# Optimization experiments

Hardware: AMD Instinct MI355X
Metric: run time of the kernel (lower is better)

The kernel has to match this reference:

```python
import jax, jax.numpy as jnp
import numpy as np

# dims: T time steps, B batch, CIN/COUT conv channels, HxW spatial, K kernel
T, B, CIN, COUT, H, Wd, K = 10, 32, 3, 64, 64, 64, 3
DECAY = 0.2      # LIF leak factor
INH = 1.625      # lateral inhibition strength (mode='threshold')


def setup_inputs() -> dict:
    key = jax.random.key(0)
    k1, k2 = jax.random.split(key)
    x = (jax.random.uniform(k1, (T, B, CIN, H, Wd)) < 0.2).astype(jnp.float32)
    W = jax.random.normal(k2, (COUT, CIN, K, K), dtype=jnp.float32)
    # normweight(): zero-mean, unit-std (biased) per output filter
    W = W - W.mean(axis=(1, 2, 3), keepdims=True)
    W = W / W.reshape(COUT, -1).std(axis=1).reshape(COUT, 1, 1, 1)
    return {"x": x, "W": W}


def _conv(x, W):
    # Conv2d stride=1, padding=1, no bias, NCHW/OIHW
    return jax.lax.conv_general_dilated(
        x, W, window_strides=(1, 1), padding=((1, 1), (1, 1)),
        dimension_numbers=("NCHW", "OIHW", "NCHW"))


def reference(x, W):
    def step(mem, x_t):
        i = _conv(x_t, W)                                        # (B,COUT,H,W)
        # ATB: adaptive per-channel threshold = max over batch+spatial
        thr = jnp.max(i, axis=(0, 2, 3), keepdims=True) + 1e-4   # (1,COUT,1,1)
        # ASF: clamp then thresholded sigmoid filter
        cur = jnp.maximum(i, 0.0)
        i_asf = thr * jax.nn.sigmoid((cur - 0.4 * thr) * (8.0 / thr))
        # LIF update with threshold = thr (set by ATB)
        mem = mem * DECAY + i_asf
        s = (mem > thr).astype(mem.dtype)                        # spikes 0/1
        # WTA k=1: keep only the strongest spiking channel per location
        score = mem * s
        winner = jnp.argmax(score, axis=1)                       # (B,H,W)
        oh = jnp.moveaxis(jax.nn.one_hot(winner, COUT, dtype=mem.dtype), -1, 1)
        s = s * oh
        # membrane reset of fired neurons
        mem = mem * (1.0 - s)
        # lateral inhibition: suppress non-winners at spiking locations
        any_sp = jnp.max(s, axis=1, keepdims=True)
        mem = mem - INH * thr * any_sp * (1.0 - s)
        return mem, s

    mem0 = jnp.zeros((B, COUT, H, Wd), jnp.float32)
    _, spikes = jax.lax.scan(step, mem0, x)
    return spikes  # (T,B,COUT,H,W)
```

## Files before the change

kernel.cpp:

```cpp
#include <hip/hip_runtime.h>
#include <math.h>

#define TT 10
#define BB 32
#define CIN 3
#define COUT 64
#define HH 64
#define WW 64
#define HW (HH*WW)
#define DECAY 0.2f
#define INH 1.625f

__device__ __forceinline__ unsigned int enc_f(float f) {
    unsigned int u = __float_as_uint(f);
    return (u & 0x80000000u) ? ~u : (u | 0x80000000u);
}
__device__ __forceinline__ float dec_f(unsigned int u) {
    u = (u & 0x80000000u) ? (u & 0x7FFFFFFFu) : ~u;
    return __uint_as_float(u);
}

__global__ __launch_bounds__(256) void thr_kernel(
    const float* __restrict__ x,
    const float* __restrict__ Wt,
    unsigned int* __restrict__ thr_raw,
    float* __restrict__ out)
{
    __shared__ float sx[CIN][6][68];
    __shared__ float wmax[4][COUT];

    const int tid  = threadIdx.x;
    const int lane = tid & 63;
    const int wave = tid >> 6;
    const int h0   = blockIdx.x * 4;
    const int b    = blockIdx.y;
    const int t    = blockIdx.z;

    float w[27];
    #pragma unroll
    for (int k = 0; k < 27; k++) w[k] = Wt[lane * 27 + k];

    const float* xb = x + ((size_t)t * BB + b) * (CIN * HW);
    for (int l = tid; l < CIN * 6 * 66; l += 256) {
        int ci  = l / 396;
        int r   = (l % 396) / 66;
        int col = l % 66;
        int gh = h0 + r - 1;
        int gw = col - 1;
        float v = 0.f;
        if (gh >= 0 && gh < HH && gw >= 0 && gw < WW)
            v = xb[ci * HW + gh * WW + gw];
        sx[ci][r][col] = v;
    }
    __syncthreads();

    float* ob = out + (((size_t)t * BB + b) * COUT) * HW;
    float mx = -INFINITY;

    for (int cc = 0; cc < 16; cc++) {
        {
            int l   = cc * 256 + tid;
            int row = l >> 4;
            int q   = l & 15;
            int c   = row >> 2;
            int hr  = row & 3;
            *(float4*)(ob + (size_t)c * HW + (h0 + hr) * WW + q * 4) =
                make_float4(0.f, 0.f, 0.f, 0.f);
        }
        float acc0 = 0.f, acc1 = 0.f, acc2 = 0.f, acc3 = 0.f;
        #pragma unroll
        for (int ci = 0; ci < CIN; ci++)
            #pragma unroll
            for (int kh = 0; kh < 3; kh++) {
                const float* rp = &sx[ci][wave + kh][cc * 4];
                float4 q = *(const float4*)rp;
                float2 r2 = *(const float2*)(rp + 4);
                float x0 = q.x, x1 = q.y, x2 = q.z, x3 = q.w;
                float x4 = r2.x, x5 = r2.y;
                const float w0 = w[ci * 9 + kh * 3 + 0];
                const float w1 = w[ci * 9 + kh * 3 + 1];
                const float w2 = w[ci * 9 + kh * 3 + 2];
                acc0 = fmaf(w0, x0, acc0); acc0 = fmaf(w1, x1, acc0); acc0 = fmaf(w2, x2, acc0);
                acc1 = fmaf(w0, x1, acc1); acc1 = fmaf(w1, x2, acc1); acc1 = fmaf(w2, x3, acc1);
                acc2 = fmaf(w0, x2, acc2); acc2 = fmaf(w1, x3, acc2); acc2 = fmaf(w2, x4, acc2);
                acc3 = fmaf(w0, x3, acc3); acc3 = fmaf(w1, x4, acc3); acc3 = fmaf(w2, x5, acc3);
            }
        mx = fmaxf(mx, fmaxf(fmaxf(acc0, acc1), fmaxf(acc2, acc3)));
    }

    wmax[wave][lane] = mx;
    __syncthreads();
    if (wave == 0) {
        float m = fmaxf(fmaxf(wmax[0][lane], wmax[1][lane]),
                        fmaxf(wmax[2][lane], wmax[3][lane]));
        atomicMax(&thr_raw[t * COUT + lane], enc_f(m));
    }
}

__global__ __launch_bounds__(256) void fused_kernel(
    const float* __restrict__ x,
    const float* __restrict__ Wt,
    const unsigned int* __restrict__ thr_raw,
    float* __restrict__ out)
{
    __shared__ float sx[5][CIN][3][24];

    const int tid  = threadIdx.x;
    const int lane = tid & 63;
    const int wave = tid >> 6;
    const int p0   = __builtin_amdgcn_readfirstlane(wave * 4);
    const int b    = blockIdx.x >> 8;
    const int h    = (blockIdx.x >> 2) & 63;
    const int w0   = (blockIdx.x & 3) << 4;

    float w[27];
    #pragma unroll
    for (int k = 0; k < 27; k++) w[k] = Wt[lane * 27 + k];

    const float* xb0 = x + (size_t)b * (CIN * HW);

#define STAGE5(T0) {                                                          \
        for (int l = tid; l < 5 * 162; l += 256) {                            \
            int t   = l / 162;                                                \
            int r0  = l - t * 162;                                            \
            int ci  = r0 / 54;                                                \
            int r1  = r0 - ci * 54;                                           \
            int r   = r1 / 18;                                                \
            int col = r1 - r * 18;                                            \
            int gh = h + r - 1;                                               \
            int gw = w0 + col - 1;                                            \
            float v = 0.f;                                                    \
            if (gh >= 0 && gh < HH && gw >= 0 && gw < WW)                     \
                v = xb0[(size_t)((T0) + t) * ((size_t)BB * CIN * HW)          \
                        + ci * HW + gh * WW + gw];                            \
            sx[t][ci][r][col] = v;                                            \
        }                                                                     \
    }

    STAGE5(0);

    float mem[4];
    #pragma unroll
    for (int j = 0; j < 4; j++) mem[j] = 0.f;

    __syncthreads();

    #pragma unroll 1
    for (int t = 0; t < TT; t++) {
        if (t == 5) {
            __syncthreads();
            STAGE5(5);
            __syncthreads();
        }
        const int slot = (t < 5) ? t : t - 5;

        float thr   = dec_f(thr_raw[t * COUT + lane]) + 1e-4f;
        float sinv  = 8.0f / thr;
        float s04   = 0.4f * thr;
        float sinh_ = INH * thr;

        int fmask = 0;

        float acc0 = 0.f, acc1 = 0.f, acc2 = 0.f, acc3 = 0.f;
        #pragma unroll
        for (int ci = 0; ci < CIN; ci++)
            #pragma unroll
            for (int kh = 0; kh < 3; kh++) {
                const float* rp = &sx[slot][ci][kh][p0];
                float4 q = *(const float4*)rp;
                float2 r2 = *(const float2*)(rp + 4);
                float x0 = q.x, x1 = q.y, x2 = q.z, x3 = q.w;
                float x4 = r2.x, x5 = r2.y;
                const float w0_ = w[ci * 9 + kh * 3 + 0];
                const float w1_ = w[ci * 9 + kh * 3 + 1];
                const float w2_ = w[ci * 9 + kh * 3 + 2];
                acc0 = fmaf(w0_, x0, acc0); acc0 = fmaf(w1_, x1, acc0); acc0 = fmaf(w2_, x2, acc0);
                acc1 = fmaf(w0_, x1, acc1); acc1 = fmaf(w1_, x2, acc1); acc1 = fmaf(w2_, x3, acc1);
                acc2 = fmaf(w0_, x2, acc2); acc2 = fmaf(w1_, x3, acc2); acc2 = fmaf(w2_, x4, acc2);
                acc3 = fmaf(w0_, x3, acc3); acc3 = fmaf(w1_, x4, acc3); acc3 = fmaf(w2_, x5, acc3);
            }

#define LIF_PX(J, ACC) {                                                    \
        float cur = fmaxf(ACC, 0.f);                                        \
        float z   = (cur - s04) * sinv;                                     \
        float sig = 1.0f / (1.0f + expf(-z));                               \
        float m   = mem[J] * DECAY + thr * sig;                             \
        int   sp  = m > thr;                                                \
        float score = sp ? m : 0.f;                                         \
        unsigned long long blt = __ballot(sp);                              \
        int fr = 0, sp_any = 0;                                             \
        if (blt) {                                  \
            float bs = score;                                               \
            int   bc = lane;                                                \
            _Pragma("unroll")                                               \
            for (int off = 32; off > 0; off >>= 1) {                        \
                float so = __shfl_xor(bs, off, 64);                         \
                int   co = __shfl_xor(bc, off, 64);                         \
                if (so > bs || (so == bs && co < bc)) { bs = so; bc = co; } \
            }                                                               \
            int spw = __shfl(sp, bc, 64);      \
            fr     = (lane == bc) && sp;                                    \
            sp_any = spw;                                                   \
        }                                                                   \
        mem[J] = fr ? 0.f : (m - (sp_any ? sinh_ : 0.f));                   \
        if (fr) fmask |= (1 << (J));                                        \
    }

        LIF_PX(0, acc0);
        LIF_PX(1, acc1);
        LIF_PX(2, acc2);
        LIF_PX(3, acc3);
#undef LIF_PX

        if (fmask) {
            float* os = out + (((size_t)t * BB + b) * COUT) * HW + h * WW + w0;
            #pragma unroll
            for (int j = 0; j < 4; j++)
                if (fmask & (1 << j))
                    os[(size_t)lane * HW + p0 + j] = 1.0f;
        }
    }
#undef STAGE5
}

extern "C" void kernel_launch(void* const* d_in, const int* in_sizes, int n_in,
                              void* d_out, int out_size, void* d_ws, size_t ws_size,
                              hipStream_t stream) {
    const float* x = (const float*)d_in[0];
    const float* W = (const float*)d_in[1];
    float* out     = (float*)d_out;

    unsigned int* thr = (unsigned int*)d_ws;
    hipMemsetAsync(thr, 0, TT * COUT * sizeof(unsigned int), stream);

    thr_kernel<<<dim3(HH / 4, BB, TT), 256, 0, stream>>>(x, W, thr, out);
    fused_kernel<<<dim3(BB * HH * 4), 256, 0, stream>>>(x, W, thr, out);
}
```

Measured before the change: 518.9 us.

## Fuse threshold and LIF passes into one cooperative kernel with grid sync

```diff
diff --git a/kernel.cpp b/kernel.cpp
--- a/kernel.cpp
+++ b/kernel.cpp
@@ -1,5 +1,8 @@
 #include <hip/hip_runtime.h>
+#include <hip/hip_cooperative_groups.h>
 #include <math.h>
+
+namespace cg = cooperative_groups;
 
 #define TT 10
 #define BB 32
@@ -10,6 +13,7 @@
 #define HW (HH*WW)
 #define DECAY 0.2f
 #define INH 1.625f
+#define NSHAD 16
 
 __device__ __forceinline__ unsigned int enc_f(float f) {
     unsigned int u = __float_as_uint(f);
@@ -20,91 +24,213 @@
     return __uint_as_float(u);
 }
 
-__global__ __launch_bounds__(256) void thr_kernel(
+__global__ __launch_bounds__(256, 4) void snn_coop(
     const float* __restrict__ x,
     const float* __restrict__ Wt,
-    unsigned int* __restrict__ thr_raw,
+    unsigned int* __restrict__ thrS,
     float* __restrict__ out)
+{
+    __shared__ float i_lds[32][256];
+    __shared__ float sx[CIN][4][68];
+    __shared__ float wmax[4][COUT];
+
+    const int tid  = threadIdx.x;
+    const int lane = tid & 63;
+    const int wave = tid >> 6;
+    const int b    = blockIdx.x >> 5;
+    const int h0   = (blockIdx.x & 31) << 1;
+    const int hr   = wave >> 1;
+    const int wb   = (wave & 1) << 5;
+    const int slot = blockIdx.x & (NSHAD - 1);
+
+    float w[27];
+    #pragma unroll
+    for (int k = 0; k < 27; k++) w[k] = Wt[lane * 27 + k];
+
+    float mem[32];
+    #pragma unroll
+    for (int j = 0; j < 32; j++) mem[j] = 0.f;
+
+    cg::grid_group grid = cg::this_grid();
+
+    const float* xb = x + (size_t)b * (CIN * HW);
+
+    #pragma unroll 1
+    for (int t = 0; t < TT; t++) {
+        for (int l = tid; l < CIN * 4 * 66; l += 256) {
+            int ci  = l / 264;
+            int r   = (l % 264) / 66;
+            int col = l % 66;
+            int gh = h0 + r - 1;
+            int gw = col - 1;
+            float v = 0.f;
+            if (gh >= 0 && gh < HH && gw >= 0 && gw < WW)
+                v = xb[(size_t)t * ((size_t)BB * CIN * HW) + ci * HW + gh * WW + gw];
+            sx[ci][r][col] = v;
+        }
+        __syncthreads();
+
+        float* ofill = out + ((size_t)t * BB + b) * ((size_t)COUT * HW);
+        float mx = -INFINITY;
+
+        #pragma unroll
+        for (int cc = 0; cc < 8; cc++) {
+            {
+                int l   = cc * 256 + tid;
+                int row = l >> 4;
+                int q   = l & 15;
+                int c   = row >> 1;
+                int hh  = row & 1;
+                *(float4*)(ofill + (size_t)c * HW + (h0 + hh) * WW + q * 4) =
+                    make_float4(0.f, 0.f, 0.f, 0.f);
+            }
+            const int c0 = wb + cc * 4;
+            float acc0 = 0.f, acc1 = 0.f, acc2 = 0.f, acc3 = 0.f;
+            #pragma unroll
+            for (int ci = 0; ci < CIN; ci++)
+                #pragma unroll
+                for (int kh = 0; kh < 3; kh++) {
+                    const float* rp = &sx[ci][hr + kh][c0];
+                    float4 q = *(const float4*)rp;
+                    float2 r2 = *(const float2*)(rp + 4);
+                    float x0 = q.x, x1 = q.y, x2 = q.z, x3 = q.w;
+                    float x4 = r2.x, x5 = r2.y;
+                    const float w0 = w[ci * 9 + kh * 3 + 0];
+                    const float w1 = w[ci * 9 + kh * 3 + 1];
+                    const float w2 = w[ci * 9 + kh * 3 + 2];
+                    acc0 = fmaf(w0, x0, acc0); acc0 = fmaf(w1, x1, acc0); acc0 = fmaf(w2, x2, acc0);
+                    acc1 = fmaf(w0, x1, acc1); acc1 = fmaf(w1, x2, acc1); acc1 = fmaf(w2, x3, acc1);
+                    acc2 = fmaf(w0, x2, acc2); acc2 = fmaf(w1, x3, acc2); acc2 = fmaf(w2, x4, acc2);
+                    acc3 = fmaf(w0, x3, acc3); acc3 = fmaf(w1, x4, acc3); acc3 = fmaf(w2, x5, acc3);
+                }
+            mx = fmaxf(mx, fmaxf(fmaxf(acc0, acc1), fmaxf(acc2, acc3)));
+            i_lds[cc * 4 + 0][tid] = acc0;
+            i_lds[cc * 4 + 1][tid] = acc1;
+            i_lds[cc * 4 + 2][tid] = acc2;
+            i_lds[cc * 4 + 3][tid] = acc3;
+        }
+
+        wmax[wave][lane] = mx;
+        __syncthreads();
+        if (wave == 0) {
+            float m = fmaxf(fmaxf(wmax[0][lane], wmax[1][lane]),
+                            fmaxf(wmax[2][lane], wmax[3][lane]));
+            atomicMax(&thrS[(t * NSHAD + slot) * COUT + lane], enc_f(m));
+        }
+
+        grid.sync();
+
+        unsigned int tm = 0;
+        #pragma unroll
+        for (int s = 0; s < NSHAD; s++) {
+            unsigned int v = thrS[(t * NSHAD + s) * COUT + lane];
+            tm = (v > tm) ? v : tm;
+        }
+        float thr   = dec_f(tm) + 1e-4f;
+        float sinv  = 8.0f / thr;
+        float s04   = 0.4f * thr;
+        float sinh_ = INH * thr;
+
+        unsigned int fmask = 0;
+
+        #pragma unroll
+        for (int j = 0; j < 32; j++) {
+            float iv  = i_lds[j][tid];
+            float cur = fmaxf(iv, 0.f);
+            float z   = (cur - s04) * sinv;
+            float sig = 1.0f / (1.0f + expf(-z));
+            float m   = mem[j] * DECAY + thr * sig;
+            int   sp  = m > thr;
+            float score = sp ? m : 0.f;
+
+            unsigned long long blt = __ballot(sp);
+            int fr = 0, sp_any = 0;
+            if (blt) {
+                float bs = score;
+                int   bc = lane;
+                #pragma unroll
+                for (int off = 32; off > 0; off >>= 1) {
+                    float so = __shfl_xor(bs, off, 64);
+                    int   co = __shfl_xor(bc, off, 64);
+                    if (so > bs || (so == bs && co < bc)) { bs = so; bc = co; }
+                }
+                int spw = __shfl(sp, bc, 64);
+                fr     = (lane == bc) && sp;
+                sp_any = spw;
+            }
+            mem[j] = fr ? 0.f : (m - (sp_any ? sinh_ : 0.f));
+            if (fr) fmask |= (1u << j);
+        }
+
+        if (fmask) {
+            float* os = out + ((size_t)t * BB + b) * ((size_t)COUT * HW)
+                      + (h0 + hr) * WW + wb;
+            #pragma unroll
+            for (int j = 0; j < 32; j++)
+                if (fmask & (1u << j))
+                    os[(size_t)lane * HW + j] = 1.0f;
+        }
+    }
+}
+
+__global__ __launch_bounds__(256) void thr_kernel(
+    const float* __restrict__ x, const float* __restrict__ Wt,
+    unsigned int* __restrict__ thr_raw, float* __restrict__ out)
 {
     __shared__ float sx[CIN][6][68];
     __shared__ float wmax[4][COUT];
-
     const int tid  = threadIdx.x;
     const int lane = tid & 63;
     const int wave = tid >> 6;
     const int h0   = blockIdx.x * 4;
     const int b    = blockIdx.y;
     const int t    = blockIdx.z;
-
     float w[27];
     #pragma unroll
     for (int k = 0; k < 27; k++) w[k] = Wt[lane * 27 + k];
-
     const float* xb = x + ((size_t)t * BB + b) * (CIN * HW);
     for (int l = tid; l < CIN * 6 * 66; l += 256) {
-        int ci  = l / 396;
-        int r   = (l % 396) / 66;
-        int col = l % 66;
-        int gh = h0 + r - 1;
-        int gw = col - 1;
+        int ci = l / 396, r = (l % 396) / 66, col = l % 66;
+        int gh = h0 + r - 1, gw = col - 1;
         float v = 0.f;
-        if (gh >= 0 && gh < HH && gw >= 0 && gw < WW)
-            v = xb[ci * HW + gh * WW + gw];
+        if (gh >= 0 && gh < HH && gw >= 0 && gw < WW) v = xb[ci * HW + gh * WW + gw];
         sx[ci][r][col] = v;
     }
     __syncthreads();
-
     float* ob = out + (((size_t)t * BB + b) * COUT) * HW;
     float mx = -INFINITY;
-
     for (int cc = 0; cc < 16; cc++) {
-        {
-            int l   = cc * 256 + tid;
-            int row = l >> 4;
-            int q   = l & 15;
-            int c   = row >> 2;
-            int hr  = row & 3;
-            *(float4*)(ob + (size_t)c * HW + (h0 + hr) * WW + q * 4) =
-                make_float4(0.f, 0.f, 0.f, 0.f);
-        }
+        { int l = cc * 256 + tid, row = l >> 4, q = l & 15, c = row >> 2, hrr = row & 3;
+          *(float4*)(ob + (size_t)c * HW + (h0 + hrr) * WW + q * 4) = make_float4(0.f,0.f,0.f,0.f); }
         float acc0 = 0.f, acc1 = 0.f, acc2 = 0.f, acc3 = 0.f;
         #pragma unroll
         for (int ci = 0; ci < CIN; ci++)
             #pragma unroll
             for (int kh = 0; kh < 3; kh++) {
                 const float* rp = &sx[ci][wave + kh][cc * 4];
-                float4 q = *(const float4*)rp;
-                float2 r2 = *(const float2*)(rp + 4);
-                float x0 = q.x, x1 = q.y, x2 = q.z, x3 = q.w;
-                float x4 = r2.x, x5 = r2.y;
-                const float w0 = w[ci * 9 + kh * 3 + 0];
-                const float w1 = w[ci * 9 + kh * 3 + 1];
-                const float w2 = w[ci * 9 + kh * 3 + 2];
-                acc0 = fmaf(w0, x0, acc0); acc0 = fmaf(w1, x1, acc0); acc0 = fmaf(w2, x2, acc0);
-                acc1 = fmaf(w0, x1, acc1); acc1 = fmaf(w1, x2, acc1); acc1 = fmaf(w2, x3, acc1);
-                acc2 = fmaf(w0, x2, acc2); acc2 = fmaf(w1, x3, acc2); acc2 = fmaf(w2, x4, acc2);
-                acc3 = fmaf(w0, x3, acc3); acc3 = fmaf(w1, x4, acc3); acc3 = fmaf(w2, x5, acc3);
+                float4 q = *(const float4*)rp; float2 r2 = *(const float2*)(rp + 4);
+                float x0=q.x,x1=q.y,x2=q.z,x3=q.w,x4=r2.x,x5=r2.y;
+                const float w0=w[ci*9+kh*3+0], w1=w[ci*9+kh*3+1], w2=w[ci*9+kh*3+2];
+                acc0=fmaf(w0,x0,acc0);acc0=fmaf(w1,x1,acc0);acc0=fmaf(w2,x2,acc0);
+                acc1=fmaf(w0,x1,acc1);acc1=fmaf(w1,x2,acc1);acc1=fmaf(w2,x3,acc1);
+                acc2=fmaf(w0,x2,acc2);acc2=fmaf(w1,x3,acc2);acc2=fmaf(w2,x4,acc2);
+                acc3=fmaf(w0,x3,acc3);acc3=fmaf(w1,x4,acc3);acc3=fmaf(w2,x5,acc3);
             }
         mx = fmaxf(mx, fmaxf(fmaxf(acc0, acc1), fmaxf(acc2, acc3)));
     }
-
     wmax[wave][lane] = mx;
     __syncthreads();
     if (wave == 0) {
-        float m = fmaxf(fmaxf(wmax[0][lane], wmax[1][lane]),
-                        fmaxf(wmax[2][lane], wmax[3][lane]));
+        float m = fmaxf(fmaxf(wmax[0][lane], wmax[1][lane]), fmaxf(wmax[2][lane], wmax[3][lane]));
         atomicMax(&thr_raw[t * COUT + lane], enc_f(m));
     }
 }
 
 __global__ __launch_bounds__(256) void fused_kernel(
-    const float* __restrict__ x,
-    const float* __restrict__ Wt,
-    const unsigned int* __restrict__ thr_raw,
-    float* __restrict__ out)
+    const float* __restrict__ x, const float* __restrict__ Wt,
+    const unsigned int* __restrict__ thr_raw, float* __restrict__ out)
 {
     __shared__ float sx[5][CIN][3][24];
-
     const int tid  = threadIdx.x;
     const int lane = tid & 63;
     const int wave = tid >> 6;
@@ -112,23 +238,15 @@
     const int b    = blockIdx.x >> 8;
     const int h    = (blockIdx.x >> 2) & 63;
     const int w0   = (blockIdx.x & 3) << 4;
-
     float w[27];
     #pragma unroll
     for (int k = 0; k < 27; k++) w[k] = Wt[lane * 27 + k];
-
     const float* xb0 = x + (size_t)b * (CIN * HW);
-
 #define STAGE5(T0) {                                                          \
         for (int l = tid; l < 5 * 162; l += 256) {                            \
-            int t   = l / 162;                                                \
-            int r0  = l - t * 162;                                            \
-            int ci  = r0 / 54;                                                \
-            int r1  = r0 - ci * 54;                                           \
-            int r   = r1 / 18;                                                \
-            int col = r1 - r * 18;                                            \
-            int gh = h + r - 1;                                               \
-            int gw = w0 + col - 1;                                            \
+            int t = l / 162, r0 = l - t * 162, ci = r0 / 54;                  \
+            int r1 = r0 - ci * 54, r = r1 / 18, col = r1 - r * 18;            \
+            int gh = h + r - 1, gw = w0 + col - 1;                            \
             float v = 0.f;                                                    \
             if (gh >= 0 && gh < HH && gw >= 0 && gw < WW)                     \
                 v = xb0[(size_t)((T0) + t) * ((size_t)BB * CIN * HW)          \
@@ -136,50 +254,32 @@
             sx[t][ci][r][col] = v;                                            \
         }                                                                     \
     }
-
     STAGE5(0);
-
     float mem[4];
     #pragma unroll
     for (int j = 0; j < 4; j++) mem[j] = 0.f;
-
     __syncthreads();
-
     #pragma unroll 1
     for (int t = 0; t < TT; t++) {
-        if (t == 5) {
-            __syncthreads();
-            STAGE5(5);
-            __syncthreads();
-        }
+        if (t == 5) { __syncthreads(); STAGE5(5); __syncthreads(); }
         const int slot = (t < 5) ? t : t - 5;
-
-        float thr   = dec_f(thr_raw[t * COUT + lane]) + 1e-4f;
-        float sinv  = 8.0f / thr;
-        float s04   = 0.4f * thr;
-        float sinh_ = INH * thr;
-
+        float thr = dec_f(thr_raw[t * COUT + lane]) + 1e-4f;
+        float sinv = 8.0f / thr, s04 = 0.4f * thr, sinh_ = INH * thr;
         int fmask = 0;
-
         float acc0 = 0.f, acc1 = 0.f, acc2 = 0.f, acc3 = 0.f;
         #pragma unroll
         for (int ci = 0; ci < CIN; ci++)
             #pragma unroll
             for (int kh = 0; kh < 3; kh++) {
                 const float* rp = &sx[slot][ci][kh][p0];
-                float4 q = *(const float4*)rp;
-                float2 r2 = *(const float2*)(rp + 4);
-                float x0 = q.x, x1 = q.y, x2 = q.z, x3 = q.w;
-                float x4 = r2.x, x5 = r2.y;
-                const float w0_ = w[ci * 9 + kh * 3 + 0];
-                const float w1_ = w[ci * 9 + kh * 3 + 1];
-                const float w2_ = w[ci * 9 + kh * 3 + 2];
-                acc0 = fmaf(w0_, x0, acc0); acc0 = fmaf(w1_, x1, acc0); acc0 = fmaf(w2_, x2, acc0);
-                acc1 = fmaf(w0_, x1, acc1); acc1 = fmaf(w1_, x2, acc1); acc1 = fmaf(w2_, x3, acc1);
-                acc2 = fmaf(w0_, x2, acc2); acc2 = fmaf(w1_, x3, acc2); acc2 = fmaf(w2_, x4, acc2);
-                acc3 = fmaf(w0_, x3, acc3); acc3 = fmaf(w1_, x4, acc3); acc3 = fmaf(w2_, x5, acc3);
+                float4 q = *(const float4*)rp; float2 r2 = *(const float2*)(rp + 4);
+                float x0=q.x,x1=q.y,x2=q.z,x3=q.w,x4=r2.x,x5=r2.y;
+                const float w0_=w[ci*9+kh*3+0], w1_=w[ci*9+kh*3+1], w2_=w[ci*9+kh*3+2];
+                acc0=fmaf(w0_,x0,acc0);acc0=fmaf(w1_,x1,acc0);acc0=fmaf(w2_,x2,acc0);
+                acc1=fmaf(w0_,x1,acc1);acc1=fmaf(w1_,x2,acc1);acc1=fmaf(w2_,x3,acc1);
+                acc2=fmaf(w0_,x2,acc2);acc2=fmaf(w1_,x3,acc2);acc2=fmaf(w2_,x4,acc2);
+                acc3=fmaf(w0_,x3,acc3);acc3=fmaf(w1_,x4,acc3);acc3=fmaf(w2_,x5,acc3);
             }
-
 #define LIF_PX(J, ACC) {                                                    \
         float cur = fmaxf(ACC, 0.f);                                        \
         float z   = (cur - s04) * sinv;                                     \
@@ -189,35 +289,27 @@
         float score = sp ? m : 0.f;                                         \
         unsigned long long blt = __ballot(sp);                              \
         int fr = 0, sp_any = 0;                                             \
-        if (blt) {                                  \
-            float bs = score;                                               \
-            int   bc = lane;                                                \
+        if (blt) {                                                          \
+            float bs = score; int bc = lane;                                \
             _Pragma("unroll")                                               \
             for (int off = 32; off > 0; off >>= 1) {                        \
                 float so = __shfl_xor(bs, off, 64);                         \
                 int   co = __shfl_xor(bc, off, 64);                         \
                 if (so > bs || (so == bs && co < bc)) { bs = so; bc = co; } \
             }                                                               \
-            int spw = __shfl(sp, bc, 64);      \
-            fr     = (lane == bc) && sp;                                    \
-            sp_any = spw;                                                   \
+            int spw = __shfl(sp, bc, 64);                                   \
+            fr = (lane == bc) && sp; sp_any = spw;                          \
         }                                                                   \
         mem[J] = fr ? 0.f : (m - (sp_any ? sinh_ : 0.f));                   \
         if (fr) fmask |= (1 << (J));                                        \
     }
-
-        LIF_PX(0, acc0);
-        LIF_PX(1, acc1);
-        LIF_PX(2, acc2);
-        LIF_PX(3, acc3);
+        LIF_PX(0, acc0); LIF_PX(1, acc1); LIF_PX(2, acc2); LIF_PX(3, acc3);
 #undef LIF_PX
-
         if (fmask) {
             float* os = out + (((size_t)t * BB + b) * COUT) * HW + h * WW + w0;
             #pragma unroll
             for (int j = 0; j < 4; j++)
-                if (fmask & (1 << j))
-                    os[(size_t)lane * HW + p0 + j] = 1.0f;
+                if (fmask & (1 << j)) os[(size_t)lane * HW + p0 + j] = 1.0f;
         }
     }
 #undef STAGE5
@@ -230,9 +322,15 @@
     const float* W = (const float*)d_in[1];
     float* out     = (float*)d_out;
 
-    unsigned int* thr = (unsigned int*)d_ws;
-    hipMemsetAsync(thr, 0, TT * COUT * sizeof(unsigned int), stream);
-
-    thr_kernel<<<dim3(HH / 4, BB, TT), 256, 0, stream>>>(x, W, thr, out);
-    fused_kernel<<<dim3(BB * HH * 4), 256, 0, stream>>>(x, W, thr, out);
-}
+    unsigned int* thrS = (unsigned int*)d_ws;
+    hipMemsetAsync(thrS, 0, TT * NSHAD * COUT * sizeof(unsigned int), stream);
+
+    void* args[] = { (void*)&x, (void*)&W, (void*)&thrS, (void*)&out };
+    hipError_t err = hipLaunchCooperativeKernel(
+        (const void*)snn_coop, dim3(BB * (HH / 2)), dim3(256), args, 0, stream);
+
+    if (err != hipSuccess) {
+        thr_kernel<<<dim3(HH / 4, BB, TT), 256, 0, stream>>>(x, W, thrS, out);
+        fused_kernel<<<dim3(BB * HH * 4), 256, 0, stream>>>(x, W, thrS, out);
+    }
+}
```

Result: slower. 1.991 ms (+283.7%).
